# Kernel optimization log

Measured on AMD Instinct MI355X. Metric: run time of the kernel, lower is better.

Reference implementation:

```python
import jax, jax.numpy as jnp
import numpy as np

Vx, Vy, B, N, C, H, M_VIEWS = 8, 8, 4, 196, 768, 12, 4
DH = C // H
SCALE = DH ** -0.5
HID = 4 * C


def _layer_norm(x, w, b, eps=1e-5):
    mu = jnp.mean(x, axis=-1, keepdims=True)
    var = jnp.mean((x - mu) ** 2, axis=-1, keepdims=True)
    return (x - mu) / jnp.sqrt(var + eps) * w + b


def setup_inputs() -> dict:
    key = jax.random.key(0)
    ks = jax.random.split(key, 32)
    s = 0.02
    inp = {
        "xs": jax.random.normal(ks[0], (Vx, B, N, C), jnp.float32),
        "ys": jax.random.normal(ks[1], (Vy, B, N, C), jnp.float32),
        "xposes": jax.random.randint(ks[2], (Vx, B, N, 2), 0, N),
        "yposes": jax.random.randint(ks[3], (Vy, B, N, 2), 0, N),
        "rel_ids": jax.random.randint(ks[4], (Vx * M_VIEWS,), 0, Vy),
        "M": M_VIEWS,
        # self-attention params (qkv_bias=False, proj has bias)
        "qkv_w": jax.random.normal(ks[5], (3 * C, C), jnp.float32) * s,
        "attn_proj_w": jax.random.normal(ks[6], (C, C), jnp.float32) * s,
        "attn_proj_b": jnp.zeros((C,), jnp.float32),
        # cross-attention params
        "q_w": jax.random.normal(ks[7], (C, C), jnp.float32) * s,
        "k_w": jax.random.normal(ks[8], (C, C), jnp.float32) * s,
        "v_w": jax.random.normal(ks[9], (C, C), jnp.float32) * s,
        "cross_proj_w": jax.random.normal(ks[10], (C, C), jnp.float32) * s,
        "cross_proj_b": jnp.zeros((C,), jnp.float32),
        # MLP
        "fc1_w": jax.random.normal(ks[11], (HID, C), jnp.float32) * s,
        "fc1_b": jnp.zeros((HID,), jnp.float32),
        "fc2_w": jax.random.normal(ks[12], (C, HID), jnp.float32) * s,
        "fc2_b": jnp.zeros((C,), jnp.float32),
        # layer norms
        "ln1_w": jnp.ones((C,), jnp.float32), "ln1_b": jnp.zeros((C,), jnp.float32),
        "ln2_w": jnp.ones((C,), jnp.float32), "ln2_b": jnp.zeros((C,), jnp.float32),
        "ln3_w": jnp.ones((C,), jnp.float32), "ln3_b": jnp.zeros((C,), jnp.float32),
        "lny_w": jnp.ones((C,), jnp.float32), "lny_b": jnp.zeros((C,), jnp.float32),
    }
    return inp


def _forward(xs, ys, rel_ids, M,
             qkv_w, attn_proj_w, attn_proj_b,
             q_w, k_w, v_w, cross_proj_w, cross_proj_b,
             fc1_w, fc1_b, fc2_w, fc2_b,
             ln1_w, ln1_b, ln2_w, ln2_b, ln3_w, ln3_b, lny_w, lny_b):
    vx, b, nx, c = xs.shape
    vy, _, ny, _ = ys.shape
    x = xs.reshape(vx * b, nx, c)

    # ---- self-attention over each target view (rope=None) ----
    h = _layer_norm(x, ln1_w, ln1_b)
    qkv = (h @ qkv_w.T).reshape(vx * b, nx, 3, H, DH)
    q = jnp.transpose(qkv[:, :, 0], (0, 2, 1, 3))  # (VB,H,N,dh)
    k = jnp.transpose(qkv[:, :, 1], (0, 2, 1, 3))
    v = jnp.transpose(qkv[:, :, 2], (0, 2, 1, 3))
    attn = jax.nn.softmax(jnp.einsum('bhnd,bhkd->bhnk', q, k) * SCALE, axis=-1)
    o = jnp.einsum('bhnk,bhkd->bnhd', attn, v).reshape(vx * b, nx, c)
    x = x + (o @ attn_proj_w.T + attn_proj_b)

    # ---- batched multi-view cross-attention ----
    xn = _layer_norm(x.reshape(vx, b, nx, c), ln2_w, ln2_b)
    yn = _layer_norm(ys, lny_w, lny_b)
    qs = (xn @ q_w.T).reshape(vx, b, nx, H, DH)
    ks = (yn @ k_w.T).reshape(vy, b, ny, H, DH)
    vs = (yn @ v_w.T).reshape(vy, b, ny, H, DH)
    ks_r = ks[rel_ids].reshape(vx, M, b, ny, H, DH)  # index_select + group
    vs_r = vs[rel_ids].reshape(vx, M, b, ny, H, DH)
    # q is broadcast across the M group dim (no materialized expand)
    scores = jnp.einsum('vbnhd,vmbkhd->vmbhnk', qs, ks_r) * SCALE
    a = jax.nn.softmax(scores, axis=-1)
    o = jnp.einsum('vmbhnk,vmbkhd->vmbnhd', a, vs_r).reshape(vx, M, b, nx, c)
    o = o @ cross_proj_w.T + cross_proj_b  # (Vx,M,B,Nx,C)
    merged = jnp.max(o, axis=1).reshape(vx * b, nx, c)  # max-merge over M
    x = x + merged

    # ---- MLP ----
    h = _layer_norm(x, ln3_w, ln3_b)
    x = x + (jax.nn.gelu(h @ fc1_w.T + fc1_b, approximate=False) @ fc2_w.T + fc2_b)
    return x.reshape(vx, b, nx, c)


def reference(xs, ys, xposes, yposes, rel_ids, M,
              qkv_w, attn_proj_w, attn_proj_b,
              q_w, k_w, v_w, cross_proj_w, cross_proj_b,
              fc1_w, fc1_b, fc2_w, fc2_b,
              ln1_w, ln1_b, ln2_w, ln2_b, ln3_w, ln3_b, lny_w, lny_b):
    # xposes/yposes unused because rope=None in this configuration
    return _forward(xs, ys, rel_ids, M,
                    qkv_w, attn_proj_w, attn_proj_b,
                    q_w, k_w, v_w, cross_proj_w, cross_proj_b,
                    fc1_w, fc1_b, fc2_w, fc2_b,
                    ln1_w, ln1_b, ln2_w, ln2_b, ln3_w, ln3_b, lny_w, lny_b)
```

## Files before the change

kernel.cpp:

```cpp
#include <hip/hip_runtime.h>
#include <hip/hip_bf16.h>
#include <stdint.h>
#include <math.h>

#define H_ 12
#define NQ 196
#define CD 768
#define HIDD 3072
#define VX 8
#define VY 8
#define BB 4
#define MV 4
#define VBB 32
#define ROWS 6272
#define CROSS_ROWS 25088
#define SCALE_LOG2E 0.180336880260608f

typedef __attribute__((ext_vector_type(8))) short short8;
typedef __attribute__((ext_vector_type(4))) float f32x4;
typedef __attribute__((ext_vector_type(4))) unsigned short u16x4;
typedef unsigned short u16;

#define AS1 __attribute__((address_space(1)))
#define AS3 __attribute__((address_space(3)))

__device__ __forceinline__ float bf2f(u16 u){
  union { unsigned int i; float f; } v; v.i = ((unsigned int)u) << 16; return v.f;
}
__device__ __forceinline__ u16 f2bf(float f){
  union { unsigned int i; float f; } v; v.f = f;
  return (u16)((v.i + 0x7fff + ((v.i >> 16) & 1)) >> 16);
}
__device__ __forceinline__ unsigned int f2u(float f){
  union { unsigned int i; float f; } v; v.f = f; return v.i;
}

struct CastSegs {
  const float* src[8];
  u16* dst[8];
  int cum[9];
};
__global__ __launch_bounds__(256) void k_cast_all(CastSegs segs){
  int i = blockIdx.x * 256 + threadIdx.x;
  if (i >= segs.cum[8]) return;
  int s = 0;
  #pragma unroll
  for (int k = 1; k < 8; k++) s += (i >= segs.cum[k]);
  const int off = i - segs.cum[s];
  segs.dst[s][off] = f2bf(segs.src[s][off]);
}

__device__ __forceinline__ void ln_row(const float* __restrict__ x,
    const float* __restrict__ w, const float* __restrict__ b,
    u16* __restrict__ out, int row, int tid){
  const float* xr = x + (size_t)row * CD;
  float v0 = xr[tid], v1 = xr[tid + 256], v2 = xr[tid + 512];
  float s  = v0 + v1 + v2;
  float s2 = v0*v0 + v1*v1 + v2*v2;
  __shared__ float red[8];
  const int lane = tid & 63, wid = tid >> 6;
  #pragma unroll
  for (int o = 32; o; o >>= 1){ s += __shfl_down(s, o); s2 += __shfl_down(s2, o); }
  if (lane == 0){ red[wid] = s; red[wid + 4] = s2; }
  __syncthreads();
  if (tid == 0){
    red[0] = red[0] + red[1] + red[2] + red[3];
    red[4] = red[4] + red[5] + red[6] + red[7];
  }
  __syncthreads();
  const float mu   = red[0] * (1.f/768.f);
  const float var  = red[4] * (1.f/768.f) - mu*mu;
  const float rstd = rsqrtf(var + 1e-5f);
  u16* orow = out + (size_t)row * CD;
  orow[tid]       = f2bf((v0 - mu)*rstd*w[tid]       + b[tid]);
  orow[tid + 256] = f2bf((v1 - mu)*rstd*w[tid + 256] + b[tid + 256]);
  orow[tid + 512] = f2bf((v2 - mu)*rstd*w[tid + 512] + b[tid + 512]);
}

__global__ __launch_bounds__(256) void k_ln_bf16(const float* __restrict__ x,
    const float* __restrict__ w, const float* __restrict__ b, u16* __restrict__ out){
  ln_row(x, w, b, out, blockIdx.x, threadIdx.x);
}

__global__ __launch_bounds__(256) void k_ln_bf16x2(
    const float* __restrict__ x0, const float* __restrict__ w0,
    const float* __restrict__ b0, u16* __restrict__ o0,
    const float* __restrict__ x1, const float* __restrict__ w1,
    const float* __restrict__ b1, u16* __restrict__ o1){
  const int bid = blockIdx.x;
  if (bid < ROWS) ln_row(x0, w0, b0, o0, bid, threadIdx.x);
  else            ln_row(x1, w1, b1, o1, bid - ROWS, threadIdx.x);
}

__global__ __launch_bounds__(256) void k_mmln(const u16* __restrict__ op,
    float* __restrict__ x, const float* __restrict__ w, const float* __restrict__ b,
    u16* __restrict__ out){
  const int row = blockIdx.x, tid = threadIdx.x;
  const int n = row % NQ, vb = row / NQ;
  const int vx = vb >> 2, bb = vb & 3;
  const size_t r0 = ((size_t)(vx * MV) * BB + bb) * NQ + n;
  const size_t ms = (size_t)BB * NQ;
  float* xr = x + (size_t)row * CD;
  float v[3], s = 0.f, s2 = 0.f;
  #pragma unroll
  for (int j = 0; j < 3; j++){
    const int col = tid + j*256;
    float mx =        bf2f(op[(r0       ) * CD + col]);
    mx = fmaxf(mx,    bf2f(op[(r0 +   ms) * CD + col]));
    mx = fmaxf(mx,    bf2f(op[(r0 + 2*ms) * CD + col]));
    mx = fmaxf(mx,    bf2f(op[(r0 + 3*ms) * CD + col]));
    const float val = xr[col] + mx;
    xr[col] = val;
    v[j] = val;
    s += val; s2 += val*val;
  }
  __shared__ float red[8];
  const int lane = tid & 63, wid = tid >> 6;
  #pragma unroll
  for (int o = 32; o; o >>= 1){ s += __shfl_down(s, o); s2 += __shfl_down(s2, o); }
  if (lane == 0){ red[wid] = s; red[wid + 4] = s2; }
  __syncthreads();
  if (tid == 0){
    red[0] = red[0] + red[1] + red[2] + red[3];
    red[4] = red[4] + red[5] + red[6] + red[7];
  }
  __syncthreads();
  const float mu   = red[0] * (1.f/768.f);
  const float var  = red[4] * (1.f/768.f) - mu*mu;
  const float rstd = rsqrtf(var + 1e-5f);
  u16* orow = out + (size_t)row * CD;
  #pragma unroll
  for (int j = 0; j < 3; j++){
    const int col = tid + j*256;
    orow[col] = f2bf((v[j] - mu)*rstd*w[col] + b[col]);
  }
}

template<int EPI, int TM, int DB>
__global__ __launch_bounds__(256) void k_gemm_bt(
    const u16* __restrict__ A, const u16* __restrict__ B,
    float* __restrict__ Cf, u16* __restrict__ Cb,
    const float* __restrict__ bias, const float* __restrict__ resid,
    int M, int N, int K){
  __shared__ u16 As[(DB + 1) * TM * 64];
  __shared__ u16 Bs[(DB + 1) * 128 * 64];
  const int tid  = threadIdx.x;
  const int lane = tid & 63;
  const int wave = tid >> 6;
  const int wr = wave >> 1, wc = wave & 1;

  const int gx = gridDim.x;
  const int nwg = gx * gridDim.y;
  const int orig = blockIdx.y * gx + blockIdx.x;
  const int q8 = nwg >> 3, r8 = nwg & 7;
  const int xcd = orig & 7, bse = orig >> 3;
  const int wg = (xcd < r8 ? xcd * (q8 + 1) : r8 * (q8 + 1) + (xcd - r8) * q8) + bse;
  const int m0 = (wg / gx) * TM, n0 = (wg % gx) * 128;

  f32x4 acc[TM/32][4];
  #pragma unroll
  for (int i = 0; i < TM/32; i++)
    #pragma unroll
    for (int j = 0; j < 4; j++) acc[i][j] = (f32x4){0.f, 0.f, 0.f, 0.f};

  const int lrow = lane >> 3;
  const int lcol = ((lane & 7) ^ lrow) * 8;
  const u16* arow = A + (size_t)(m0 + wave*(TM/4) + lrow) * K + lcol;
  const u16* brow = B + (size_t)(n0 + wave*32 + lrow) * K + lcol;

  auto STG = [&](int nb, int k0){
    #pragma unroll
    for (int i = 0; i < TM/32; i++)
      __builtin_amdgcn_global_load_lds(
        (const AS1 void*)(arow + (size_t)i*8*K + k0),
        (AS3 void*)(As + nb*TM*64 + (wave*(TM/4) + i*8)*64), 16, 0, 0);
    #pragma unroll
    for (int i = 0; i < 4; i++)
      __builtin_amdgcn_global_load_lds(
        (const AS1 void*)(brow + (size_t)i*8*K + k0),
        (AS3 void*)(Bs + nb*128*64 + (wave*32 + i*8)*64), 16, 0, 0);
  };

  auto COMPUTE = [&](int nb){
    const u16* ab = As + nb*TM*64 + (wr*(TM/2) + (lane & 15))*64;
    const u16* bb = Bs + nb*128*64 + (wc*64 + (lane & 15))*64;
    const int r7 = lane & 7;
    #pragma unroll
    for (int kk = 0; kk < 2; kk++){
      const int sl = (((lane >> 4) + 4*kk) ^ r7) * 8;
      short8 af[TM/32], bfr[4];
      #pragma unroll
      for (int f = 0; f < TM/32; f++) af[f] = *(const short8*)(ab + f*1024 + sl);
      #pragma unroll
      for (int f = 0; f < 4; f++)     bfr[f] = *(const short8*)(bb + f*1024 + sl);
      #pragma unroll
      for (int i = 0; i < TM/32; i++)
        #pragma unroll
        for (int j = 0; j < 4; j++)
          acc[i][j] = __builtin_amdgcn_mfma_f32_16x16x32_bf16(af[i], bfr[j], acc[i][j], 0, 0, 0);
    }
  };

  if (DB){
    const int NT = K >> 6;
    STG(0, 0);
    __syncthreads();
    for (int it = 0; it < NT; ++it){
      const int cb = it & 1;
      if (it + 1 < NT) STG(cb ^ 1, (it + 1) * 64);
      COMPUTE(cb);
      __syncthreads();
    }
  } else {
    for (int k0 = 0; k0 < K; k0 += 64){
      STG(0, k0);
      __syncthreads();
      COMPUTE(0);
      __syncthreads();
    }
  }

  #pragma unroll
  for (int i = 0; i < TM/32; i++){
    const int rb = m0 + wr*(TM/2) + i*16 + (lane >> 4)*4;
    #pragma unroll
    for (int j = 0; j < 4; j++){
      const int col = n0 + wc*64 + j*16 + (lane & 15);
      #pragma unroll
      for (int r = 0; r < 4; r++){
        const size_t idx = (size_t)(rb + r) * N + col;
        const float v = acc[i][j][r];
        if (EPI == 0){
          Cb[idx] = f2bf(v);
        } else if (EPI == 1){
          Cf[idx] = v + bias[col] + resid[idx];
        } else if (EPI == 2){
          Cf[idx] = v + bias[col];
        } else if (EPI == 3){
          float g = v + bias[col];
          g = 0.5f * g * (1.f + erff(g * 0.70710678118654752f));
          Cb[idx] = f2bf(g);
        } else if (EPI == 4){
          Cb[idx] = f2bf(v + bias[col]);
        } else {
          Cb[idx] = f2bf(col < 768 ? v * SCALE_LOG2E : v);
        }
      }
    }
  }
}

template<int MODE>
__global__ __launch_bounds__(256) void k_attn_mfma(
    const u16* __restrict__ Qb, const u16* __restrict__ Kb, const u16* __restrict__ Vb,
    u16* __restrict__ Ob, const int* __restrict__ rel_ids){
  __shared__ u16 Kl[2][2048];
  __shared__ u16 Vl[2][2048];

  size_t qbase, kbase, vbase, obase;
  int qstr, kstr;
  if (MODE == 0){
    const int vb = blockIdx.x / H_, h = blockIdx.x % H_;
    qbase = (size_t)vb * NQ * 2304 + h * 64; qstr = 2304;
    kbase = qbase + 768; vbase = qbase + 1536; kstr = 2304;
    obase = (size_t)vb * NQ * CD + h * 64;
  } else {
    const int h = blockIdx.x % H_; int t = blockIdx.x / H_;
    const int b = t % BB; t /= BB;
    const int m = t % MV; const int vx = t / MV;
    const int rel = rel_ids[vx * MV + m];
    qbase = ((size_t)(vx * BB + b) * NQ) * CD + h * 64; qstr = CD;
    kbase = ((size_t)(rel * BB + b) * NQ) * 1536 + h * 64; kstr = 1536;
    vbase = kbase + 768;
    obase = ((size_t)((vx * MV + m) * BB + b) * NQ) * CD + h * 64;
  }

  const int tid  = threadIdx.x;
  const int lane = tid & 63;
  const int wave = tid >> 6;
  const int lq   = lane & 15;
  const int g    = lane >> 4;

  short8 qfrag[4][2];
  #pragma unroll
  for (int qf = 0; qf < 4; qf++){
    int qrow = wave*64 + qf*16 + lq; if (qrow > 195) qrow = 195;
    const u16* qp = Qb + qbase + (size_t)qrow * qstr + g*8;
    qfrag[qf][0] = *(const short8*)(qp);
    qfrag[qf][1] = *(const short8*)(qp + 32);
  }

  union U8 { unsigned u[4]; short8 s; };

  f32x4 oacc[4][4];
  #pragma unroll
  for (int i = 0; i < 4; i++)
    #pragma unroll
    for (int j = 0; j < 4; j++) oacc[i][j] = (f32x4){0.f,0.f,0.f,0.f};
  f32x4 lacc[4];
  #pragma unroll
  for (int i = 0; i < 4; i++) lacc[i] = (f32x4){0.f,0.f,0.f,0.f};
  U8 ones;
  #pragma unroll
  for (int i = 0; i < 4; i++) ones.u[i] = 0x3F803F80u;

  const int skey  = tid >> 3;
  const int sslot = (tid & 7) ^ (skey & 7);
  const int vkey = lane >> 1;
  const int vdh  = wave*16 + (lane & 1)*8;

  auto STAGE = [&](int nb, int t0n){
    int kg = t0n + skey; if (kg > 195) kg = 195;
    __builtin_amdgcn_global_load_lds(
        (const AS1 void*)(Kb + kbase + (size_t)kg*kstr + sslot*8),
        (AS3 void*)(&Kl[nb][wave*512]), 16, 0, 0);
    int vg = t0n + vkey; if (vg > 195) vg = 195;
    __builtin_amdgcn_global_load_lds(
        (const AS1 void*)(Vb + vbase + (size_t)vg*kstr + vdh),
        (AS3 void*)(&Vl[nb][wave*512]), 16, 0, 0);
  };

  STAGE(0, 0);
  __syncthreads();

  for (int t = 0; t < 7; t++){
    const int cb = t & 1;
    const int t0 = t * 32;
    if (t < 6) STAGE(cb ^ 1, t0 + 32);

    f32x4 sacc[4][2];
    #pragma unroll
    for (int qf = 0; qf < 4; qf++)
      #pragma unroll
      for (int kf = 0; kf < 2; kf++) sacc[qf][kf] = (f32x4){0.f,0.f,0.f,0.f};
    __builtin_amdgcn_s_setprio(1);
    #pragma unroll
    for (int kf = 0; kf < 2; kf++){
      const int key = kf*16 + lq;
      #pragma unroll
      for (int ks = 0; ks < 2; ks++){
        short8 kfrag = *(const short8*)(&Kl[cb][key*64 + (((ks<<2) + g) ^ (key & 7))*8]);
        #pragma unroll
        for (int qf = 0; qf < 4; qf++)
          sacc[qf][kf] = __builtin_amdgcn_mfma_f32_16x16x32_bf16(kfrag, qfrag[qf][ks], sacc[qf][kf], 0, 0, 0);
      }
    }
    __builtin_amdgcn_s_setprio(0);

    const AS3 u16* vp = (const AS3 u16*)(&Vl[cb][0]) + (size_t)lane*4;
    uint2 tr0a, tr0b, tr1a, tr1b, tr2a, tr2b, tr3a, tr3b;
    asm volatile("ds_read_b64_tr_b16 %0, %1 offset:0"    : "=&v"(tr0a) : "v"(vp));
    asm volatile("ds_read_b64_tr_b16 %0, %1 offset:512"  : "=&v"(tr0b) : "v"(vp));
    asm volatile("ds_read_b64_tr_b16 %0, %1 offset:1024" : "=&v"(tr1a) : "v"(vp));
    asm volatile("ds_read_b64_tr_b16 %0, %1 offset:1536" : "=&v"(tr1b) : "v"(vp));
    asm volatile("ds_read_b64_tr_b16 %0, %1 offset:2048" : "=&v"(tr2a) : "v"(vp));
    asm volatile("ds_read_b64_tr_b16 %0, %1 offset:2560" : "=&v"(tr2b) : "v"(vp));
    asm volatile("ds_read_b64_tr_b16 %0, %1 offset:3072" : "=&v"(tr3a) : "v"(vp));
    asm volatile("ds_read_b64_tr_b16 %0, %1 offset:3584" : "=&v"(tr3b) : "v"(vp));

    short8 vfrag[4];
    #pragma unroll
    for (int qf = 0; qf < 4; qf++){
      float p[8];
      #pragma unroll
      for (int kf = 0; kf < 2; kf++)
        #pragma unroll
        for (int r = 0; r < 4; r++)
          p[kf*4 + r] = exp2f(sacc[qf][kf][r]);
      if (t == 6){
        #pragma unroll
        for (int kf = 0; kf < 2; kf++)
          #pragma unroll
          for (int r = 0; r < 4; r++)
            if (192 + kf*16 + g*4 + r >= NQ) p[kf*4 + r] = 0.f;
      }
      U8 pk;
      pk.u[0] = (f2u(p[0]) >> 16) | (f2u(p[1]) & 0xffff0000u);
      pk.u[1] = (f2u(p[2]) >> 16) | (f2u(p[3]) & 0xffff0000u);
      pk.u[2] = (f2u(p[4]) >> 16) | (f2u(p[5]) & 0xffff0000u);
      pk.u[3] = (f2u(p[6]) >> 16) | (f2u(p[7]) & 0xffff0000u);

      if (qf == 0){
        asm volatile("s_waitcnt lgkmcnt(0)" ::: "memory");
        __builtin_amdgcn_sched_barrier(0);
        U8 v0; v0.u[0]=tr0a.x; v0.u[1]=tr0a.y; v0.u[2]=tr0b.x; v0.u[3]=tr0b.y; vfrag[0]=v0.s;
        U8 v1; v1.u[0]=tr1a.x; v1.u[1]=tr1a.y; v1.u[2]=tr1b.x; v1.u[3]=tr1b.y; vfrag[1]=v1.s;
        U8 v2; v2.u[0]=tr2a.x; v2.u[1]=tr2a.y; v2.u[2]=tr2b.x; v2.u[3]=tr2b.y; vfrag[2]=v2.s;
        U8 v3; v3.u[0]=tr3a.x; v3.u[1]=tr3a.y; v3.u[2]=tr3b.x; v3.u[3]=tr3b.y; vfrag[3]=v3.s;
      }
      __builtin_amdgcn_s_setprio(1);
      #pragma unroll
      for (int dhf = 0; dhf < 4; dhf++)
        oacc[qf][dhf] = __builtin_amdgcn_mfma_f32_16x16x32_bf16(vfrag[dhf], pk.s, oacc[qf][dhf], 0, 0, 0);
      lacc[qf] = __builtin_amdgcn_mfma_f32_16x16x32_bf16(ones.s, pk.s, lacc[qf], 0, 0, 0);
      __builtin_amdgcn_s_setprio(0);
    }
    __syncthreads();
  }

  #pragma unroll
  for (int qf = 0; qf < 4; qf++){
    const int qrow = wave*64 + qf*16 + lq;
    if (qrow < 196){
      const float inv = 1.f / lacc[qf][0];
      u16* orow = Ob + obase + (size_t)qrow * CD;
      #pragma unroll
      for (int dhf = 0; dhf < 4; dhf++){
        uint2 pk;
        pk.x = (unsigned)f2bf(oacc[qf][dhf][0]*inv) | ((unsigned)f2bf(oacc[qf][dhf][1]*inv) << 16);
        pk.y = (unsigned)f2bf(oacc[qf][dhf][2]*inv) | ((unsigned)f2bf(oacc[qf][dhf][3]*inv) << 16);
        *(uint2*)(orow + dhf*16 + g*4) = pk;
      }
    }
  }
}

extern "C" void kernel_launch(void* const* d_in, const int* in_sizes, int n_in,
                              void* d_out, int out_size, void* d_ws, size_t ws_size,
                              hipStream_t stream){
  const float* xs           = (const float*)d_in[0];
  const float* ys           = (const float*)d_in[1];
  const int*   rel_ids      = (const int*)  d_in[4];
  const float* qkv_w        = (const float*)d_in[6];
  const float* attn_proj_w  = (const float*)d_in[7];
  const float* attn_proj_b  = (const float*)d_in[8];
  const float* q_w          = (const float*)d_in[9];
  const float* k_w          = (const float*)d_in[10];
  const float* v_w          = (const float*)d_in[11];
  const float* cross_proj_w = (const float*)d_in[12];
  const float* cross_proj_b = (const float*)d_in[13];
  const float* fc1_w        = (const float*)d_in[14];
  const float* fc1_b        = (const float*)d_in[15];
  const float* fc2_w        = (const float*)d_in[16];
  const float* fc2_b        = (const float*)d_in[17];
  const float* ln1_w        = (const float*)d_in[18];
  const float* ln1_b        = (const float*)d_in[19];
  const float* ln2_w        = (const float*)d_in[20];
  const float* ln2_b        = (const float*)d_in[21];
  const float* ln3_w        = (const float*)d_in[22];
  const float* ln3_b        = (const float*)d_in[23];
  const float* lny_w        = (const float*)d_in[24];
  const float* lny_b        = (const float*)d_in[25];
  float* out = (float*)d_out;

  char* ws = (char*)d_ws;
  size_t off = 0;
  auto alloc = [&](size_t bytes) -> char* {
    char* p = ws + off; off += (bytes + 255) & ~(size_t)255; return p;
  };
  u16* wb_qkv   = (u16*)alloc((size_t)2304*768*2);
  u16* wb_aproj = (u16*)alloc((size_t)768*768*2);
  u16* wb_q     = (u16*)alloc((size_t)768*768*2);
  u16* wb_kv    = (u16*)alloc((size_t)1536*768*2);
  u16* wb_cproj = (u16*)alloc((size_t)768*768*2);
  u16* wb_fc1   = (u16*)alloc((size_t)3072*768*2);
  u16* wb_fc2   = (u16*)alloc((size_t)768*3072*2);
  float* x_ws   = (float*)alloc((size_t)ROWS*CD*4);
  u16* hbuf     = (u16*)alloc((size_t)ROWS*CD*2);
  u16* ynbuf    = (u16*)alloc((size_t)ROWS*CD*2);
  u16* o_self   = (u16*)alloc((size_t)ROWS*CD*2);
  u16* qs       = (u16*)alloc((size_t)ROWS*CD*2);
  u16* kvs      = (u16*)alloc((size_t)ROWS*1536*2);
  u16* o_cross  = (u16*)alloc((size_t)CROSS_ROWS*CD*2);
  char* un = alloc((size_t)CROSS_ROWS*CD*2);
  u16* qkvbuf = (u16*)un;
  u16* oproj  = (u16*)un;
  u16* mid    = (u16*)un;

  CastSegs segs;
  const float* srcs[8] = {qkv_w, attn_proj_w, q_w, k_w, v_w, cross_proj_w, fc1_w, fc2_w};
  u16* dsts[8] = {wb_qkv, wb_aproj, wb_q, wb_kv, wb_kv + 768*768, wb_cproj, wb_fc1, wb_fc2};
  int lens[8]  = {2304*768, 768*768, 768*768, 768*768, 768*768, 768*768, 3072*768, 3072*768};
  segs.cum[0] = 0;
  for (int i = 0; i < 8; i++){ segs.src[i] = srcs[i]; segs.dst[i] = dsts[i];
                               segs.cum[i+1] = segs.cum[i] + lens[i]; }
  k_cast_all<<<(segs.cum[8] + 255) / 256, 256, 0, stream>>>(segs);

  k_ln_bf16<<<ROWS, 256, 0, stream>>>(xs, ln1_w, ln1_b, hbuf);
  k_gemm_bt<5,128,1><<<dim3(2304/128, ROWS/128), 256, 0, stream>>>(
      hbuf, wb_qkv, nullptr, qkvbuf, nullptr, nullptr, ROWS, 2304, 768);
  k_attn_mfma<0><<<VBB * H_, 256, 0, stream>>>(qkvbuf, qkvbuf, qkvbuf, o_self, rel_ids);
  k_gemm_bt<1,64,1><<<dim3(768/128, ROWS/64), 256, 0, stream>>>(
      o_self, wb_aproj, x_ws, nullptr, attn_proj_b, xs, ROWS, 768, 768);

  k_ln_bf16x2<<<2*ROWS, 256, 0, stream>>>(x_ws, ln2_w, ln2_b, hbuf,
                                          ys, lny_w, lny_b, ynbuf);
  k_gemm_bt<5,64,1><<<dim3(768/128, ROWS/64), 256, 0, stream>>>(
      hbuf, wb_q, nullptr, qs, nullptr, nullptr, ROWS, 768, 768);
  k_gemm_bt<0,128,1><<<dim3(1536/128, ROWS/128), 256, 0, stream>>>(
      ynbuf, wb_kv, nullptr, kvs, nullptr, nullptr, ROWS, 1536, 768);
  k_attn_mfma<1><<<VX * MV * BB * H_, 256, 0, stream>>>(qs, kvs, kvs, o_cross, rel_ids);
  k_gemm_bt<4,128,1><<<dim3(768/128, CROSS_ROWS/128), 256, 0, stream>>>(
      o_cross, wb_cproj, nullptr, oproj, cross_proj_b, nullptr, CROSS_ROWS, 768, 768);
  k_mmln<<<ROWS, 256, 0, stream>>>(oproj, x_ws, ln3_w, ln3_b, hbuf);

  k_gemm_bt<3,128,1><<<dim3(HIDD/128, ROWS/128), 256, 0, stream>>>(
      hbuf, wb_fc1, nullptr, mid, fc1_b, nullptr, ROWS, HIDD, 768);
  k_gemm_bt<1,64,1><<<dim3(768/128, ROWS/64), 256, 0, stream>>>(
      mid, wb_fc2, out, nullptr, fc2_b, x_ws, ROWS, 768, HIDD);
}
```

Baseline: 376.4 us.

## Fuse cross-attention projection with max-merge over views into one GEMM

Adds a GEMM kernel that computes the cross projection for all four M views of each output row tile at once, keeping four accumulator sets and reducing them with max in the epilogue before adding bias and the residual in place. This removes the bf16 write and re-read of the 25088x768 projected tensor and the separate max-merge kernel, leaving a plain layer norm afterwards. In exchange it holds four times the accumulators per thread, which raises register pressure, and it skips the intermediate bf16 rounding of the projection before the max.

```diff
diff --git a/kernel.cpp b/kernel.cpp
--- a/kernel.cpp
+++ b/kernel.cpp
@@ -90,50 +90,6 @@
   const int bid = blockIdx.x;
   if (bid < ROWS) ln_row(x0, w0, b0, o0, bid, threadIdx.x);
   else            ln_row(x1, w1, b1, o1, bid - ROWS, threadIdx.x);
-}
-
-__global__ __launch_bounds__(256) void k_mmln(const u16* __restrict__ op,
-    float* __restrict__ x, const float* __restrict__ w, const float* __restrict__ b,
-    u16* __restrict__ out){
-  const int row = blockIdx.x, tid = threadIdx.x;
-  const int n = row % NQ, vb = row / NQ;
-  const int vx = vb >> 2, bb = vb & 3;
-  const size_t r0 = ((size_t)(vx * MV) * BB + bb) * NQ + n;
-  const size_t ms = (size_t)BB * NQ;
-  float* xr = x + (size_t)row * CD;
-  float v[3], s = 0.f, s2 = 0.f;
-  #pragma unroll
-  for (int j = 0; j < 3; j++){
-    const int col = tid + j*256;
-    float mx =        bf2f(op[(r0       ) * CD + col]);
-    mx = fmaxf(mx,    bf2f(op[(r0 +   ms) * CD + col]));
-    mx = fmaxf(mx,    bf2f(op[(r0 + 2*ms) * CD + col]));
-    mx = fmaxf(mx,    bf2f(op[(r0 + 3*ms) * CD + col]));
-    const float val = xr[col] + mx;
-    xr[col] = val;
-    v[j] = val;
-    s += val; s2 += val*val;
-  }
-  __shared__ float red[8];
-  const int lane = tid & 63, wid = tid >> 6;
-  #pragma unroll
-  for (int o = 32; o; o >>= 1){ s += __shfl_down(s, o); s2 += __shfl_down(s2, o); }
-  if (lane == 0){ red[wid] = s; red[wid + 4] = s2; }
-  __syncthreads();
-  if (tid == 0){
-    red[0] = red[0] + red[1] + red[2] + red[3];
-    red[4] = red[4] + red[5] + red[6] + red[7];
-  }
-  __syncthreads();
-  const float mu   = red[0] * (1.f/768.f);
-  const float var  = red[4] * (1.f/768.f) - mu*mu;
-  const float rstd = rsqrtf(var + 1e-5f);
-  u16* orow = out + (size_t)row * CD;
-  #pragma unroll
-  for (int j = 0; j < 3; j++){
-    const int col = tid + j*256;
-    orow[col] = f2bf((v[j] - mu)*rstd*w[col] + b[col]);
-  }
 }
 
 template<int EPI, int TM, int DB>
@@ -245,6 +201,99 @@
         } else {
           Cb[idx] = f2bf(col < 768 ? v * SCALE_LOG2E : v);
         }
+      }
+    }
+  }
+}
+
+__global__ __launch_bounds__(256) void k_cpmax(
+    const u16* __restrict__ A, const u16* __restrict__ B,
+    const float* __restrict__ bias, float* __restrict__ xw, int K){
+  __shared__ u16 As[4][4096];
+  __shared__ u16 Bs[8192];
+  const int tid = threadIdx.x, lane = tid & 63, wave = tid >> 6;
+  const int wr = wave >> 1, wc = wave & 1;
+
+  const int gx = gridDim.x;
+  const int nwg = gx * gridDim.y;
+  const int orig = blockIdx.y * gx + blockIdx.x;
+  const int q8 = nwg >> 3, r8 = nwg & 7;
+  const int xcd = orig & 7, bse = orig >> 3;
+  const int wg = (xcd < r8 ? xcd * (q8 + 1) : r8 * (q8 + 1) + (xcd - r8) * q8) + bse;
+  const int m0 = (wg / gx) * 64, n0 = (wg % gx) * 128;
+
+  f32x4 acc[4][2][4];
+  #pragma unroll
+  for (int m = 0; m < 4; m++)
+    #pragma unroll
+    for (int i = 0; i < 2; i++)
+      #pragma unroll
+      for (int j = 0; j < 4; j++) acc[m][i][j] = (f32x4){0.f,0.f,0.f,0.f};
+
+  const int lrow = lane >> 3;
+  const int lcol = ((lane & 7) ^ lrow) * 8;
+  const int r0 = m0 + wave*16 + lrow;
+  const int r1 = r0 + 8;
+  const int vb0 = r0 / NQ, n0q = r0 - vb0 * NQ;
+  const int vb1 = r1 / NQ, n1q = r1 - vb1 * NQ;
+  const int ib0 = (((vb0 >> 2) << 4) + (vb0 & 3)) * NQ + n0q;
+  const int ib1 = (((vb1 >> 2) << 4) + (vb1 & 3)) * NQ + n1q;
+  const u16* a0 = A + (size_t)ib0 * K + lcol;
+  const u16* a1 = A + (size_t)ib1 * K + lcol;
+  const u16* brow = B + (size_t)(n0 + wave*32 + lrow) * K + lcol;
+  const size_t mstep = (size_t)(BB * NQ) * K;
+
+  for (int k0 = 0; k0 < K; k0 += 64){
+    #pragma unroll
+    for (int m = 0; m < 4; m++){
+      __builtin_amdgcn_global_load_lds(
+        (const AS1 void*)(a0 + (size_t)m*mstep + k0),
+        (AS3 void*)(As[m] + (wave*16)*64), 16, 0, 0);
+      __builtin_amdgcn_global_load_lds(
+        (const AS1 void*)(a1 + (size_t)m*mstep + k0),
+        (AS3 void*)(As[m] + (wave*16 + 8)*64), 16, 0, 0);
+    }
+    #pragma unroll
+    for (int i = 0; i < 4; i++)
+      __builtin_amdgcn_global_load_lds(
+        (const AS1 void*)(brow + (size_t)i*8*K + k0),
+        (AS3 void*)(Bs + (wave*32 + i*8)*64), 16, 0, 0);
+    __syncthreads();
+    const int r7 = lane & 7;
+    const int abase = (wr*32 + (lane & 15))*64;
+    const u16* bb = Bs + (wc*64 + (lane & 15))*64;
+    #pragma unroll
+    for (int kk = 0; kk < 2; kk++){
+      const int sl = (((lane >> 4) + 4*kk) ^ r7) * 8;
+      short8 bfr[4];
+      #pragma unroll
+      for (int f = 0; f < 4; f++) bfr[f] = *(const short8*)(bb + f*1024 + sl);
+      #pragma unroll
+      for (int m = 0; m < 4; m++){
+        short8 af0 = *(const short8*)(As[m] + abase + sl);
+        short8 af1 = *(const short8*)(As[m] + abase + 1024 + sl);
+        #pragma unroll
+        for (int j = 0; j < 4; j++){
+          acc[m][0][j] = __builtin_amdgcn_mfma_f32_16x16x32_bf16(af0, bfr[j], acc[m][0][j], 0, 0, 0);
+          acc[m][1][j] = __builtin_amdgcn_mfma_f32_16x16x32_bf16(af1, bfr[j], acc[m][1][j], 0, 0, 0);
+        }
+      }
+    }
+    __syncthreads();
+  }
+
+  #pragma unroll
+  for (int i = 0; i < 2; i++){
+    const int rb = m0 + wr*32 + i*16 + (lane >> 4)*4;
+    #pragma unroll
+    for (int j = 0; j < 4; j++){
+      const int col = n0 + wc*64 + j*16 + (lane & 15);
+      #pragma unroll
+      for (int r = 0; r < 4; r++){
+        const float v = fmaxf(fmaxf(acc[0][i][j][r], acc[1][i][j][r]),
+                              fmaxf(acc[2][i][j][r], acc[3][i][j][r]));
+        const size_t idx = (size_t)(rb + r) * CD + col;
+        xw[idx] += v + bias[col];
       }
     }
   }
@@ -464,7 +513,6 @@
   u16* o_cross  = (u16*)alloc((size_t)CROSS_ROWS*CD*2);
   char* un = alloc((size_t)CROSS_ROWS*CD*2);
   u16* qkvbuf = (u16*)un;
-  u16* oproj  = (u16*)un;
   u16* mid    = (u16*)un;
 
   CastSegs segs;
@@ -490,9 +538,9 @@
   k_gemm_bt<0,128,1><<<dim3(1536/128, ROWS/128), 256, 0, stream>>>(
       ynbuf, wb_kv, nullptr, kvs, nullptr, nullptr, ROWS, 1536, 768);
   k_attn_mfma<1><<<VX * MV * BB * H_, 256, 0, stream>>>(qs, kvs, kvs, o_cross, rel_ids);
-  k_gemm_bt<4,128,1><<<dim3(768/128, CROSS_ROWS/128), 256, 0, stream>>>(
-      o_cross, wb_cproj, nullptr, oproj, cross_proj_b, nullptr, CROSS_ROWS, 768, 768);
-  k_mmln<<<ROWS, 256, 0, stream>>>(oproj, x_ws, ln3_w, ln3_b, hbuf);
+  k_cpmax<<<dim3(768/128, ROWS/64), 256, 0, stream>>>(
+      o_cross, wb_cproj, cross_proj_b, x_ws, 768);
+  k_ln_bf16<<<ROWS, 256, 0, stream>>>(x_ws, ln3_w, ln3_b, hbuf);
 
   k_gemm_bt<3,128,1><<<dim3(HIDD/128, ROWS/128), 256, 0, stream>>>(
       hbuf, wb_fc1, nullptr, mid, fc1_b, nullptr, ROWS, HIDD, 768);
```

Result: slower. 398.2 us (+5.8%).
